# Kernel optimization log

Hardware: AMD Instinct MI355X
Metric: run time of the kernel (lower is better)

The kernel has to match this reference:

```python
import jax, jax.numpy as jnp
import numpy as np

# Model dims
T0 = 2048      # tokens (batch*seq flattened)
D = 2048       # hidden_size
E = 256        # n_routed_experts
K = 8          # num_experts_per_tok
G = 8          # expert groups
EG = 32        # experts per group
R = 64         # tucker rank
I = 1408       # moe_intermediate_size


def setup_inputs() -> dict:
    key = jax.random.key(0)
    ks = jax.random.split(key, 12)
    f = lambda k, s: jax.random.normal(k, s, dtype=jnp.float32) * 0.02
    return {
        "hidden_states": jax.random.normal(ks[0], (T0, D), dtype=jnp.float32),
        "w_gate": f(ks[1], (D, E)),
        # Tucker factors per group: shared in-factor A, per-expert core C, shared out-factor B
        "A_gate": f(ks[2], (G, D, R)), "C_gate": f(ks[3], (G, EG, R, R)), "B_gate": f(ks[4], (G, R, I)),
        "A_up":   f(ks[5], (G, D, R)), "C_up":   f(ks[6], (G, EG, R, R)), "B_up":   f(ks[7], (G, R, I)),
        "A_down": f(ks[8], (G, I, R)), "C_down": f(ks[9], (G, EG, R, R)), "B_down": f(ks[10], (G, R, D)),
    }


def _tucker(x, A, C, B, inner):
    # x: [T, d_in], A: [d_in, R], C: [EG, R, R] gathered per-token, B: [R, d_out]
    h1 = x @ A                                    # [T, R]
    h2 = jnp.einsum('tr,trs->ts', h1, C[inner])   # per-token expert core
    return h2 @ B                                 # [T, d_out]


def reference(hidden_states, w_gate, A_gate, C_gate, B_gate,
              A_up, C_up, B_up, A_down, C_down, B_down):
    # Router: softmax in fp32, top-k, renormalize
    logits = hidden_states @ w_gate                              # [T0, E]
    probs = jax.nn.softmax(logits.astype(jnp.float32), axis=-1)
    rw, sel = jax.lax.top_k(probs, K)                            # [T0, K]
    rw = (rw / rw.sum(axis=-1, keepdims=True)).astype(hidden_states.dtype)

    idx = sel.reshape(-1)          # [T0*K] expert ids of dispatched rows
    gid = idx // EG                # group id
    inner = idx % EG               # expert within group
    x = jnp.repeat(hidden_states, K, axis=0)   # repeat_interleave dispatch [T0*K, D]

    out = jnp.zeros_like(x)
    for g in range(G):             # static loop over 8 structurally distinct groups
        m = (gid == g)[:, None]
        xg = jnp.where(m, x, 0.0)  # masked dispatch (zeros flow to zero through the MLP)
        go = _tucker(xg, A_gate[g], C_gate[g], B_gate[g], inner)
        uo = _tucker(xg, A_up[g],   C_up[g],   B_up[g],   inner)
        inter = jax.nn.silu(go) * uo
        do = _tucker(inter, A_down[g], C_down[g], B_down[g], inner)
        out = out + jnp.where(m, do, 0.0)

    # weighted combine
    return (out.reshape(T0, K, D) * rw[..., None]).sum(axis=1)
```

## Files before the change

### kernel.cpp

```cpp
#include <hip/hip_runtime.h>
#include <math.h>

constexpr int T0n = 2048;
constexpr int Dn  = 2048;
constexpr int En  = 256;
constexpr int Gn  = 8;
constexpr int EGn = 32;
constexpr int Rn  = 64;
constexpr int In  = 1408;

constexpr int NROWS = T0n * 8;
constexpr int SEGCAP = NROWS;
constexpr int KS_R = 4;

typedef __attribute__((ext_vector_type(8))) short s8v;
typedef __attribute__((ext_vector_type(4))) float f4v;
typedef __attribute__((ext_vector_type(4))) int i4v;
#define MFMA16(a, b, c) __builtin_amdgcn_mfma_f32_16x16x32_bf16(a, b, c, 0, 0, 0)
#define MFMAI8(a, b, c) __builtin_amdgcn_mfma_i32_16x16x64_i8(a, b, c, 0, 0, 0)

__device__ __forceinline__ unsigned short f2bf(float x) {
  unsigned int u = __float_as_uint(x);
  unsigned int r = (u + 0x7FFFu + ((u >> 16) & 1u)) >> 16;
  return (unsigned short)r;
}

struct TD { const float* src; unsigned short* dst; int rows, cols, nbx, per_batch, base; };
struct TD9 { TD t[9]; };

__global__ __launch_bounds__(256) void k_tcvt9(TD9 D) {
  __shared__ float tbuf[32][33];
  int id = blockIdx.x;
  int ti = 0;
#pragma unroll
  for (int i = 1; i < 9; ++i) ti = (id >= D.t[i].base) ? i : ti;
  TD d = D.t[ti];
  int local = id - d.base;
  int bz = local / d.per_batch;
  int rem = local - bz * d.per_batch;
  int by = rem / d.nbx;
  int bx = rem - by * d.nbx;

  size_t boff = (size_t)bz * d.rows * d.cols;
  const float* src = d.src + boff;
  unsigned short* dst = d.dst + boff;
  int c0 = bx * 32, r0 = by * 32;
  int tx = threadIdx.x & 31, ty = threadIdx.x >> 5;
  for (int i = ty; i < 32; i += 8)
    tbuf[i][tx] = src[(size_t)(r0 + i) * d.cols + c0 + tx];
  __syncthreads();
  for (int i = ty; i < 32; i += 8)
    dst[(size_t)(c0 + i) * d.rows + r0 + tx] = f2bf(tbuf[tx][i]);
}

__device__ __forceinline__ int4 limbs4(float v, double sc) {
  double d = (double)v * sc;
  d = fmin(fmax(d, -2.0e9), 2.0e9);
  int x = __double2int_rn(d);
  int l0 = (int)(signed char)(x & 0xff); x = (x - l0) >> 8;
  int l1 = (int)(signed char)(x & 0xff); x = (x - l1) >> 8;
  int l2 = (int)(signed char)(x & 0xff); x = (x - l2) >> 8;
  return make_int4(l0, l1, l2, x);
}

__global__ __launch_bounds__(256) void k_quant_h(
    const float* __restrict__ H, char* __restrict__ hq) {
  const size_t PL = (size_t)T0n * Dn;
  size_t i = (size_t)blockIdx.x * 256 + threadIdx.x;
  float4 v = *(const float4*)&H[i * 4];
  int4 a = limbs4(v.x, 268435456.0);
  int4 b = limbs4(v.y, 268435456.0);
  int4 c = limbs4(v.z, 268435456.0);
  int4 d = limbs4(v.w, 268435456.0);
  unsigned int p0 = (a.x & 0xff) | ((b.x & 0xff) << 8) | ((c.x & 0xff) << 16) | ((unsigned)(d.x & 0xff) << 24);
  unsigned int p1 = (a.y & 0xff) | ((b.y & 0xff) << 8) | ((c.y & 0xff) << 16) | ((unsigned)(d.y & 0xff) << 24);
  unsigned int p2 = (a.z & 0xff) | ((b.z & 0xff) << 8) | ((c.z & 0xff) << 16) | ((unsigned)(d.z & 0xff) << 24);
  unsigned int p3 = (a.w & 0xff) | ((b.w & 0xff) << 8) | ((c.w & 0xff) << 16) | ((unsigned)(d.w & 0xff) << 24);
  *(unsigned int*)&hq[0 * PL + i * 4] = p0;
  *(unsigned int*)&hq[1 * PL + i * 4] = p1;
  *(unsigned int*)&hq[2 * PL + i * 4] = p2;
  *(unsigned int*)&hq[3 * PL + i * 4] = p3;
}

__global__ __launch_bounds__(256) void k_quant_wT(
    const float* __restrict__ W, char* __restrict__ wqT) {
  __shared__ float tb[32][33];
  const size_t PL = (size_t)En * Dn;
  int kb = blockIdx.x * 32, nb = blockIdx.y * 32;
  int tx = threadIdx.x & 31, ty = threadIdx.x >> 5;
  for (int i = ty; i < 32; i += 8)
    tb[i][tx] = W[(size_t)(kb + i) * En + nb + tx];
  __syncthreads();
  for (int i = ty; i < 32; i += 8) {
    int4 l = limbs4(tb[tx][i], 8589934592.0);
    size_t off = (size_t)(nb + i) * Dn + kb + tx;
    wqT[0 * PL + off] = (char)l.x;
    wqT[1 * PL + off] = (char)l.y;
    wqT[2 * PL + off] = (char)l.z;
    wqT[3 * PL + off] = (char)l.w;
  }
}

__global__ __launch_bounds__(256) void k_router_i8(
    const char* __restrict__ hq, const char* __restrict__ wqT,
    float* __restrict__ part) {
  __shared__ __align__(16) char Asl[4][64][80];
  __shared__ __align__(16) char Bsl[4][64][80];
  const int n0 = blockIdx.x * 64, m0 = blockIdx.y * 64;
  const int kc = blockIdx.z;
  const int tid = threadIdx.x;
  const int w = tid >> 6, ln = tid & 63;
  const int quad = ln >> 4, lane16 = ln & 15;

  const char* ha = hq + ((size_t)w * T0n + m0 + ln) * Dn;
  const char* ba = wqT + ((size_t)w * En + n0 + ln) * Dn;

  i4v acc[4][5] = {};

  const int kbeg = kc * (Dn / KS_R);
  for (int k0 = kbeg; k0 < kbeg + Dn / KS_R; k0 += 64) {
#pragma unroll
    for (int q = 0; q < 4; ++q) {
      *(uint4*)&Asl[w][ln][q * 16] = *(const uint4*)&ha[k0 + q * 16];
      *(uint4*)&Bsl[w][ln][q * 16] = *(const uint4*)&ba[k0 + q * 16];
    }
    __syncthreads();
    i4v b0 = *(const i4v*)&Bsl[0][w * 16 + lane16][quad * 16];
    i4v b1 = *(const i4v*)&Bsl[1][w * 16 + lane16][quad * 16];
    i4v b2 = *(const i4v*)&Bsl[2][w * 16 + lane16][quad * 16];
    i4v b3 = *(const i4v*)&Bsl[3][w * 16 + lane16][quad * 16];
#pragma unroll
    for (int mt = 0; mt < 4; ++mt) {
      i4v a0 = *(const i4v*)&Asl[0][mt * 16 + lane16][quad * 16];
      i4v a1 = *(const i4v*)&Asl[1][mt * 16 + lane16][quad * 16];
      i4v a2 = *(const i4v*)&Asl[2][mt * 16 + lane16][quad * 16];
      i4v a3 = *(const i4v*)&Asl[3][mt * 16 + lane16][quad * 16];
      acc[mt][0] = MFMAI8(a0, b2, acc[mt][0]);
      acc[mt][0] = MFMAI8(a1, b1, acc[mt][0]);
      acc[mt][0] = MFMAI8(a2, b0, acc[mt][0]);
      acc[mt][1] = MFMAI8(a0, b3, acc[mt][1]);
      acc[mt][1] = MFMAI8(a1, b2, acc[mt][1]);
      acc[mt][1] = MFMAI8(a2, b1, acc[mt][1]);
      acc[mt][1] = MFMAI8(a3, b0, acc[mt][1]);
      acc[mt][2] = MFMAI8(a1, b3, acc[mt][2]);
      acc[mt][2] = MFMAI8(a2, b2, acc[mt][2]);
      acc[mt][2] = MFMAI8(a3, b1, acc[mt][2]);
      acc[mt][3] = MFMAI8(a2, b3, acc[mt][3]);
      acc[mt][3] = MFMAI8(a3, b2, acc[mt][3]);
      acc[mt][4] = MFMAI8(a3, b3, acc[mt][4]);
    }
    __syncthreads();
  }

  float* prow = part + (size_t)kc * T0n * En;
#pragma unroll
  for (int mt = 0; mt < 4; ++mt)
#pragma unroll
    for (int r = 0; r < 4; ++r) {
      int row = m0 + mt * 16 + quad * 4 + r;
      int col = n0 + w * 16 + lane16;
      double v = (double)acc[mt][0][r] * 0x1p-45 +
                 (double)acc[mt][1][r] * 0x1p-37 +
                 (double)acc[mt][2][r] * 0x1p-29 +
                 (double)acc[mt][3][r] * 0x1p-21 +
                 (double)acc[mt][4][r] * 0x1p-13;
      prow[(size_t)row * En + col] = (float)v;
    }
}

__global__ __launch_bounds__(256) void k_topk(
    const float* __restrict__ part, int* __restrict__ sel,
    float* __restrict__ rw, int* __restrict__ cnt_e) {
  const int wid = threadIdx.x >> 6, ln = threadIdx.x & 63;
  const int t = blockIdx.x * 4 + wid;

  double v[4];
#pragma unroll
  for (int j = 0; j < 4; ++j) {
    double s = 0.0;
#pragma unroll
    for (int kc = 0; kc < KS_R; ++kc)
      s += (double)part[((size_t)kc * T0n + t) * En + ln + 64 * j];
    v[j] = s;
  }

  float topv[8];
  int topi[8];
#pragma unroll
  for (int k = 0; k < 8; ++k) {
    double bv = v[0]; int bi = ln;
#pragma unroll
    for (int j = 1; j < 4; ++j) {
      int cand = ln + 64 * j;
      if (v[j] > bv || (v[j] == bv && cand < bi)) { bv = v[j]; bi = cand; }
    }
#pragma unroll
    for (int off = 32; off > 0; off >>= 1) {
      double ov = __shfl_xor(bv, off);
      int oi = __shfl_xor(bi, off);
      if (ov > bv || (ov == bv && oi < bi)) { bv = ov; bi = oi; }
    }
    topv[k] = (float)bv; topi[k] = bi;
    if ((bi & 63) == ln) v[bi >> 6] = -1e300;
  }

  if (ln < 8) {
    float m = topv[0];
    float ssum = 0.f;
#pragma unroll
    for (int k = 0; k < 8; ++k) ssum += expf(topv[k] - m);
    rw[t * 8 + ln] = expf(topv[ln] - m) / ssum;
    sel[t * 8 + ln] = topi[ln];
    atomicAdd(&cnt_e[topi[ln]], 1);
  }
}

__global__ __launch_bounds__(256) void k_scan(
    const int* __restrict__ cnt_e, int* __restrict__ off_e,
    int* __restrict__ cur_e, int* __restrict__ grp_n) {
  __shared__ int c[256];
  int tid = threadIdx.x;
  c[tid] = cnt_e[tid];
  __syncthreads();
  int g = tid >> 5, ei = tid & 31;
  int run = 0;
  for (int i = 0; i < ei; ++i) run += c[(g << 5) + i];
  off_e[tid] = g * SEGCAP + run;
  cur_e[tid] = g * SEGCAP + run;
  if (ei == 31) grp_n[g] = run + c[tid];
}

__global__ void k_scatter(const int* __restrict__ sel, int* __restrict__ cur_e,
                          int* __restrict__ rseg) {
  int i = blockIdx.x * 256 + threadIdx.x;
  int e = sel[i];
  int pos = atomicAdd(&cur_e[e], 1);
  rseg[pos] = i;
}

__global__ __launch_bounds__(512) void k_h1_mfma(
    const float* __restrict__ H,
    const unsigned short* __restrict__ AgT, const unsigned short* __restrict__ AuT,
    unsigned short* __restrict__ h1gb, unsigned short* __restrict__ h1ub) {
  const int t0 = blockIdx.x * 64;
  const int g = blockIdx.y;
  const unsigned short* Wg = AgT + (size_t)g * Rn * Dn;
  const unsigned short* Wu = AuT + (size_t)g * Rn * Dn;

  __shared__ unsigned short As[64 * 72];
  __shared__ unsigned short Bg_l[64 * 72];
  __shared__ unsigned short Bu_l[64 * 72];
  const int tid = threadIdx.x;
  const int w = tid >> 6, ln = tid & 63;
  const int path = w >> 2, ws = w & 3;
  const int quad = ln >> 4, lane16 = ln & 15;
  const int j = tid >> 3, q = (tid & 7) * 8;

  f4v S[4] = {};

  for (int k0 = 0; k0 < Dn; k0 += 64) {
    {
      float4 v0 = *(const float4*)&H[(size_t)(t0 + j) * Dn + k0 + q];
      float4 v1 = *(const float4*)&H[(size_t)(t0 + j) * Dn + k0 + q + 4];
      ushort4 o0, o1;
      o0.x = f2bf(v0.x); o0.y = f2bf(v0.y); o0.z = f2bf(v0.z); o0.w = f2bf(v0.w);
      o1.x = f2bf(v1.x); o1.y = f2bf(v1.y); o1.z = f2bf(v1.z); o1.w = f2bf(v1.w);
      *(ushort4*)&As[j * 72 + q] = o0;
      *(ushort4*)&As[j * 72 + q + 4] = o1;
      *(uint4*)&Bg_l[j * 72 + q] = *(const uint4*)&Wg[(size_t)j * Dn + k0 + q];
      *(uint4*)&Bu_l[j * 72 + q] = *(const uint4*)&Wu[(size_t)j * Dn + k0 + q];
    }
    __syncthreads();
    const unsigned short* Bl = path ? Bu_l : Bg_l;
#pragma unroll
    for (int kk = 0; kk < 2; ++kk) {
      s8v a = *(const s8v*)&As[(ws * 16 + lane16) * 72 + kk * 32 + quad * 8];
#pragma unroll
      for (int nt = 0; nt < 4; ++nt) {
        s8v b = *(const s8v*)&Bl[(nt * 16 + lane16) * 72 + kk * 32 + quad * 8];
        S[nt] = MFMA16(a, b, S[nt]);
      }
    }
    __syncthreads();
  }
  unsigned short* out = path ? h1ub : h1gb;
#pragma unroll
  for (int nt = 0; nt < 4; ++nt)
#pragma unroll
    for (int r = 0; r < 4; ++r) {
      int row = t0 + ws * 16 + quad * 4 + r;
      int col = g * 64 + nt * 16 + lane16;
      out[(size_t)row * (Gn * Rn) + col] = f2bf(S[nt][r]);
    }
}

__global__ __launch_bounds__(512) void k_core_gu(
    const unsigned short* __restrict__ h1gb, const unsigned short* __restrict__ h1ub,
    const unsigned short* __restrict__ CgT, const unsigned short* __restrict__ CuT,
    const int* __restrict__ rseg, const int* __restrict__ off_e,
    const int* __restrict__ cnt_e,
    unsigned short* __restrict__ h2gb, unsigned short* __restrict__ h2ub) {
  const int e = blockIdx.x;
  const int ne = cnt_e[e];
  if (ne == 0) return;
  const int g = e >> 5;
  const int base = off_e[e];
  __shared__ unsigned short Cg_l[64 * 72];
  __shared__ unsigned short Cu_l[64 * 72];
  __shared__ unsigned short Ags[64 * 72];
  __shared__ unsigned short Aus[64 * 72];
  __shared__ int rids[64];
  const int tid = threadIdx.x;
  const int w = tid >> 6, ln = tid & 63;
  const int path = w >> 2, ws = w & 3;
  const int quad = ln >> 4, lane16 = ln & 15;
  const int j = tid >> 3, q = (tid & 7) * 8;
  {
    const unsigned short* cg = CgT + (size_t)e * (Rn * Rn);
    const unsigned short* cu = CuT + (size_t)e * (Rn * Rn);
    *(uint4*)&Cg_l[j * 72 + q] = *(const uint4*)&cg[j * 64 + q];
    *(uint4*)&Cu_l[j * 72 + q] = *(const uint4*)&cu[j * 64 + q];
  }
  const int ntile = (ne + 63) >> 6;
  for (int it = 0; it < ntile; ++it) {
    int mi = it * 64 + j;
    int rid = (mi < ne) ? rseg[base + mi] : -1;
    if ((tid & 7) == 0) rids[j] = rid;
    uint4 zg = {0, 0, 0, 0}, zu = {0, 0, 0, 0};
    if (rid >= 0) {
      zg = *(const uint4*)&h1gb[(size_t)(rid >> 3) * (Gn * Rn) + g * 64 + q];
      zu = *(const uint4*)&h1ub[(size_t)(rid >> 3) * (Gn * Rn) + g * 64 + q];
    }
    *(uint4*)&Ags[j * 72 + q] = zg;
    *(uint4*)&Aus[j * 72 + q] = zu;
    __syncthreads();
    const unsigned short* Al = path ? Aus : Ags;
    const unsigned short* Cl = path ? Cu_l : Cg_l;
    f4v S[4] = {};
#pragma unroll
    for (int kk = 0; kk < 2; ++kk) {
      s8v a = *(const s8v*)&Al[(ws * 16 + lane16) * 72 + kk * 32 + quad * 8];
#pragma unroll
      for (int nt = 0; nt < 4; ++nt) {
        s8v b = *(const s8v*)&Cl[(nt * 16 + lane16) * 72 + kk * 32 + quad * 8];
        S[nt] = MFMA16(a, b, S[nt]);
      }
    }
    unsigned short* out = path ? h2ub : h2gb;
#pragma unroll
    for (int nt = 0; nt < 4; ++nt)
#pragma unroll
      for (int r = 0; r < 4; ++r) {
        int rid2 = rids[ws * 16 + quad * 4 + r];
        if (rid2 >= 0)
          out[(size_t)rid2 * 64 + nt * 16 + lane16] = f2bf(S[nt][r]);
      }
    __syncthreads();
  }
}

__global__ __launch_bounds__(256) void k_expand_mfma(
    const unsigned short* __restrict__ h2gb, const unsigned short* __restrict__ h2ub,
    const unsigned short* __restrict__ BgT, const unsigned short* __restrict__ BuT,
    const unsigned short* __restrict__ AdT,
    const int* __restrict__ rseg, const int* __restrict__ grp_n,
    float* __restrict__ h1d) {
  const int g = blockIdx.z;
  const int ng = grp_n[g];
  const int m0 = blockIdx.y * 128;
  if (m0 >= ng) return;
  const int c_beg = blockIdx.x * 6;
  const int c_end = min(22, c_beg + 6);

  __shared__ unsigned short Hg_l[128 * 72];
  __shared__ unsigned short Hu_l[128 * 72];
  __shared__ unsigned short Bg_l[64 * 72];
  __shared__ unsigned short Bu_l[64 * 72];
  __shared__ unsigned short Ad_l[64 * 72];
  __shared__ int rids[128];

  const int tid = threadIdx.x;
  const int w = tid >> 6, ln = tid & 63;
  const int quad = ln >> 4, lane16 = ln & 15;

  if (tid < 128) rids[tid] = (m0 + tid < ng) ? rseg[g * SEGCAP + m0 + tid] : -1;
  __syncthreads();
#pragma unroll
  for (int i = 0; i < 4; ++i) {
    int c = tid + i * 256;
    int row = c >> 3, cc = (c & 7) * 8;
    int rid = rids[row];
    uint4 zg = {0, 0, 0, 0}, zu = {0, 0, 0, 0};
    if (rid >= 0) {
      zg = *(const uint4*)&h2gb[(size_t)rid * 64 + cc];
      zu = *(const uint4*)&h2ub[(size_t)rid * 64 + cc];
    }
    *(uint4*)&Hg_l[row * 72 + cc] = zg;
    *(uint4*)&Hu_l[row * 72 + cc] = zu;
  }

  const unsigned short* Bg_base = BgT + (size_t)g * In * Rn;
  const unsigned short* Bu_base = BuT + (size_t)g * In * Rn;
  const unsigned short* Ad_base = AdT + (size_t)g * Rn * In;

  f4v P[2][4] = {};

  for (int c = c_beg; c < c_end; ++c) {
    const int i0 = c * 64;
#pragma unroll
    for (int i = 0; i < 2; ++i) {
      int cq = tid + i * 256;
      int row = cq >> 3, co = (cq & 7) * 8;
      *(uint4*)&Bg_l[row * 72 + co] = *(const uint4*)&Bg_base[(size_t)(i0 + row) * Rn + co];
      *(uint4*)&Bu_l[row * 72 + co] = *(const uint4*)&Bu_base[(size_t)(i0 + row) * Rn + co];
      *(uint4*)&Ad_l[row * 72 + co] = *(const uint4*)&Ad_base[(size_t)row * In + i0 + co];
    }
    __syncthreads();

    f4v Sg[2][4] = {}, Su[2][4] = {};
#pragma unroll
    for (int kk = 0; kk < 2; ++kk) {
      s8v ag[2], au[2], bg[4], bu[4];
#pragma unroll
      for (int mt = 0; mt < 2; ++mt) {
        ag[mt] = *(const s8v*)&Hg_l[(w * 32 + mt * 16 + lane16) * 72 + kk * 32 + quad * 8];
        au[mt] = *(const s8v*)&Hu_l[(w * 32 + mt * 16 + lane16) * 72 + kk * 32 + quad * 8];
      }
#pragma unroll
      for (int nt = 0; nt < 4; ++nt) {
        bg[nt] = *(const s8v*)&Bg_l[(nt * 16 + lane16) * 72 + kk * 32 + quad * 8];
        bu[nt] = *(const s8v*)&Bu_l[(nt * 16 + lane16) * 72 + kk * 32 + quad * 8];
      }
#pragma unroll
      for (int mt = 0; mt < 2; ++mt)
#pragma unroll
        for (int nt = 0; nt < 4; ++nt) {
          Sg[mt][nt] = MFMA16(ag[mt], bg[nt], Sg[mt][nt]);
          Su[mt][nt] = MFMA16(au[mt], bu[nt], Su[mt][nt]);
        }
    }
    __syncthreads();
    {
      unsigned short* ibuf = (w < 2) ? Bg_l : Bu_l;
#pragma unroll
      for (int mt = 0; mt < 2; ++mt)
#pragma unroll
        for (int nt = 0; nt < 4; ++nt)
#pragma unroll
          for (int r = 0; r < 4; ++r) {
            float sg = Sg[mt][nt][r];
            float v = sg / (1.f + __expf(-sg)) * Su[mt][nt][r];
            int row = (w * 32 + mt * 16 + quad * 4 + r) & 63;
            ibuf[row * 72 + nt * 16 + lane16] = f2bf(v);
          }
    }
    __syncthreads();
#pragma unroll
    for (int kk = 0; kk < 2; ++kk) {
      s8v ai[2], bd[4];
#pragma unroll
      for (int mt = 0; mt < 2; ++mt) {
        const unsigned short* src = (w < 2) ? Bg_l : Bu_l;
        int arow = (w * 32 + mt * 16 + lane16) & 63;
        ai[mt] = *(const s8v*)&src[arow * 72 + kk * 32 + quad * 8];
      }
#pragma unroll
      for (int nt = 0; nt < 4; ++nt)
        bd[nt] = *(const s8v*)&Ad_l[(nt * 16 + lane16) * 72 + kk * 32 + quad * 8];
#pragma unroll
      for (int mt = 0; mt < 2; ++mt)
#pragma unroll
        for (int nt = 0; nt < 4; ++nt)
          P[mt][nt] = MFMA16(ai[mt], bd[nt], P[mt][nt]);
    }
    __syncthreads();
  }

#pragma unroll
  for (int mt = 0; mt < 2; ++mt)
#pragma unroll
    for (int nt = 0; nt < 4; ++nt)
#pragma unroll
      for (int r = 0; r < 4; ++r) {
        int lrow = w * 32 + mt * 16 + quad * 4 + r;
        int rid = rids[lrow];
        if (rid >= 0)
          atomicAdd(&h1d[(size_t)rid * 64 + nt * 16 + lane16], P[mt][nt][r]);
      }
}

__global__ __launch_bounds__(512) void k_core_down(
    const float* __restrict__ h1d, const unsigned short* __restrict__ CdT,
    const float* __restrict__ rw,
    const int* __restrict__ rseg, const int* __restrict__ off_e,
    const int* __restrict__ cnt_e,
    float* __restrict__ y) {
  const int e = blockIdx.x;
  const int ne = cnt_e[e];
  if (ne == 0) return;
  const int g = e >> 5;
  const int base = off_e[e];
  __shared__ unsigned short Bd_l[64 * 72];
  __shared__ unsigned short Ad_l[128 * 72];
  __shared__ int rids[128];
  const int tid = threadIdx.x;
  const int w = tid >> 6, ln = tid & 63;
  const int quad = ln >> 4, lane16 = ln & 15;
  {
    int j = tid >> 3, q = (tid & 7) * 8;
    const unsigned short* cd = CdT + (size_t)e * (Rn * Rn);
    *(uint4*)&Bd_l[j * 72 + q] = *(const uint4*)&cd[j * 64 + q];
  }
  const int gj = tid >> 2, gq = (tid & 3) * 16;
  const int ntile = (ne + 127) >> 7;
  for (int it = 0; it < ntile; ++it) {
    int mi = it * 128 + gj;
    int rid = (mi < ne) ? rseg[base + mi] : -1;
    if ((tid & 3) == 0) rids[gj] = rid;
#pragma unroll
    for (int i = 0; i < 4; ++i) {
      int kb = gq + i * 4;
      float4 vd = {0.f, 0.f, 0.f, 0.f};
      if (rid >= 0) vd = *(const float4*)&h1d[(size_t)rid * 64 + kb];
      ushort4 od;
      od.x = f2bf(vd.x); od.y = f2bf(vd.y); od.z = f2bf(vd.z); od.w = f2bf(vd.w);
      *(ushort4*)&Ad_l[gj * 72 + kb] = od;
    }
    __syncthreads();
    f4v Sd[4] = {};
#pragma unroll
    for (int kk = 0; kk < 2; ++kk) {
      s8v ad = *(const s8v*)&Ad_l[(w * 16 + lane16) * 72 + kk * 32 + quad * 8];
#pragma unroll
      for (int nt = 0; nt < 4; ++nt) {
        s8v bd = *(const s8v*)&Bd_l[(nt * 16 + lane16) * 72 + kk * 32 + quad * 8];
        Sd[nt] = MFMA16(ad, bd, Sd[nt]);
      }
    }
#pragma unroll
    for (int nt = 0; nt < 4; ++nt)
#pragma unroll
      for (int r = 0; r < 4; ++r) {
        int rid2 = rids[w * 16 + quad * 4 + r];
        if (rid2 >= 0) {
          float wgt = rw[rid2];
          atomicAdd(&y[(size_t)(rid2 >> 3) * (Gn * Rn) + g * 64 + nt * 16 + lane16],
                    wgt * Sd[nt][r]);
        }
      }
    __syncthreads();
  }
}

__global__ __launch_bounds__(256) void k_combine(
    const float* __restrict__ y, const unsigned short* __restrict__ BdT,
    float* __restrict__ outp) {
  const int t0 = blockIdx.y * 128, n0 = blockIdx.x * 128;
  __shared__ unsigned short As[128 * 72];
  __shared__ unsigned short Bs[128 * 72];
  const int tid = threadIdx.x;
  const int w = tid >> 6, ln = tid & 63;
  const int quad = ln >> 4, lane16 = ln & 15;
  const int mbase = (w >> 1) * 64, nbase = (w & 1) * 64;

  f4v acc[4][4] = {};

  for (int k0 = 0; k0 < Gn * Rn; k0 += 64) {
#pragma unroll
    for (int i = 0; i < 8; ++i) {
      int c = tid + i * 256;
      int row = c >> 4, cc = (c & 15) * 4;
      float4 v = *(const float4*)&y[(size_t)(t0 + row) * (Gn * Rn) + k0 + cc];
      ushort4 o;
      o.x = f2bf(v.x); o.y = f2bf(v.y); o.z = f2bf(v.z); o.w = f2bf(v.w);
      *(ushort4*)&As[row * 72 + cc] = o;
    }
#pragma unroll
    for (int i = 0; i < 4; ++i) {
      int c = tid + i * 256;
      int row = c >> 3, cc = (c & 7) * 8;
      *(uint4*)&Bs[row * 72 + cc] = *(const uint4*)&BdT[(size_t)(n0 + row) * (Gn * Rn) + k0 + cc];
    }
    __syncthreads();
#pragma unroll
    for (int kk = 0; kk < 2; ++kk) {
      s8v a[4], b[4];
#pragma unroll
      for (int mt = 0; mt < 4; ++mt)
        a[mt] = *(const s8v*)&As[(mbase + mt * 16 + lane16) * 72 + kk * 32 + quad * 8];
#pragma unroll
      for (int nt = 0; nt < 4; ++nt)
        b[nt] = *(const s8v*)&Bs[(nbase + nt * 16 + lane16) * 72 + kk * 32 + quad * 8];
#pragma unroll
      for (int mt = 0; mt < 4; ++mt)
#pragma unroll
        for (int nt = 0; nt < 4; ++nt)
          acc[mt][nt] = MFMA16(a[mt], b[nt], acc[mt][nt]);
    }
    __syncthreads();
  }
#pragma unroll
  for (int mt = 0; mt < 4; ++mt)
#pragma unroll
    for (int nt = 0; nt < 4; ++nt)
#pragma unroll
      for (int r = 0; r < 4; ++r)
        outp[(size_t)(t0 + mbase + mt * 16 + quad * 4 + r) * Dn +
             n0 + nbase + nt * 16 + lane16] = acc[mt][nt][r];
}

extern "C" void kernel_launch(void* const* d_in, const int* in_sizes, int n_in,
                              void* d_out, int out_size, void* d_ws, size_t ws_size,
                              hipStream_t stream) {
  const float* hidden = (const float*)d_in[0];
  const float* w_gate = (const float*)d_in[1];
  const float* A_gate = (const float*)d_in[2];
  const float* C_gate = (const float*)d_in[3];
  const float* B_gate = (const float*)d_in[4];
  const float* A_up   = (const float*)d_in[5];
  const float* C_up   = (const float*)d_in[6];
  const float* B_up   = (const float*)d_in[7];
  const float* A_down = (const float*)d_in[8];
  const float* C_down = (const float*)d_in[9];
  const float* B_down = (const float*)d_in[10];
  float* out = (float*)d_out;

  char* base = (char*)d_ws;
  size_t o = 0;
  unsigned short* h2gb = (unsigned short*)(base + o); o += (size_t)NROWS * Rn * 2;
  unsigned short* h2ub = (unsigned short*)(base + o); o += (size_t)NROWS * Rn * 2;
  unsigned short* AgT  = (unsigned short*)(base + o); o += (size_t)Gn * Rn * Dn * 2;
  unsigned short* AuT  = (unsigned short*)(base + o); o += (size_t)Gn * Rn * Dn * 2;
  unsigned short* BgT  = (unsigned short*)(base + o); o += (size_t)Gn * In * Rn * 2;
  unsigned short* BuT  = (unsigned short*)(base + o); o += (size_t)Gn * In * Rn * 2;
  unsigned short* AdT  = (unsigned short*)(base + o); o += (size_t)Gn * Rn * In * 2;
  unsigned short* BdT  = (unsigned short*)(base + o); o += (size_t)Dn * Gn * Rn * 2;
  unsigned short* CgT  = (unsigned short*)(base + o); o += (size_t)En * Rn * Rn * 2;
  unsigned short* CuT  = (unsigned short*)(base + o); o += (size_t)En * Rn * Rn * 2;
  unsigned short* CdT  = (unsigned short*)(base + o); o += (size_t)En * Rn * Rn * 2;
  unsigned short* h1gb = (unsigned short*)(base + o); o += (size_t)T0n * Gn * Rn * 2;
  unsigned short* h1ub = (unsigned short*)(base + o); o += (size_t)T0n * Gn * Rn * 2;
  float* h1d = (float*)(base + o); o += (size_t)NROWS * Rn * 4;
  float* y   = (float*)(base + o); o += (size_t)T0n * Gn * Rn * 4;
  float* rwp = (float*)(base + o); o += (size_t)NROWS * 4;
  int* sel   = (int*)(base + o); o += (size_t)NROWS * 4;
  int* rseg  = (int*)(base + o); o += (size_t)Gn * SEGCAP * 4;
  int* cnt_e = (int*)(base + o); o += En * 4;
  int* off_e = (int*)(base + o); o += En * 4;
  int* cur_e = (int*)(base + o); o += En * 4;
  int* grp_n = (int*)(base + o); o += Gn * 4;
  float* part = (float*)base;
  char* hq  = base + (size_t)KS_R * T0n * En * 4;
  char* wqT = hq + (size_t)4 * T0n * Dn;

  hipMemsetAsync(cnt_e, 0, En * sizeof(int), stream);

  k_quant_h<<<T0n * Dn / 1024, 256, 0, stream>>>(hidden, hq);
  k_quant_wT<<<dim3(Dn / 32, En / 32), 256, 0, stream>>>(w_gate, wqT);
  k_router_i8<<<dim3(En / 64, T0n / 64, KS_R), 256, 0, stream>>>(hq, wqT, part);
  k_topk<<<T0n / 4, 256, 0, stream>>>(part, sel, rwp, cnt_e);
  k_scan<<<1, 256, 0, stream>>>(cnt_e, off_e, cur_e, grp_n);
  k_scatter<<<NROWS / 256, 256, 0, stream>>>(sel, cur_e, rseg);

  hipMemsetAsync(h1d, 0, (size_t)NROWS * Rn * sizeof(float), stream);
  hipMemsetAsync(y,   0, (size_t)T0n * Gn * Rn * sizeof(float), stream);

  {
    TD9 D;
    D.t[0] = {A_gate, AgT, Dn, Rn, Rn / 32, (Rn / 32) * (Dn / 32), 0};
    D.t[1] = {A_up,   AuT, Dn, Rn, Rn / 32, (Rn / 32) * (Dn / 32), 1024};
    D.t[2] = {B_gate, BgT, Rn, In, In / 32, (In / 32) * (Rn / 32), 2048};
    D.t[3] = {B_up,   BuT, Rn, In, In / 32, (In / 32) * (Rn / 32), 2752};
    D.t[4] = {A_down, AdT, In, Rn, Rn / 32, (Rn / 32) * (In / 32), 3456};
    D.t[5] = {B_down, BdT, Gn * Rn, Dn, Dn / 32, (Dn / 32) * (Gn * Rn / 32), 4160};
    D.t[6] = {C_gate, CgT, Rn, Rn, 2, 4, 5184};
    D.t[7] = {C_up,   CuT, Rn, Rn, 2, 4, 6208};
    D.t[8] = {C_down, CdT, Rn, Rn, 2, 4, 7232};
    k_tcvt9<<<8256, 256, 0, stream>>>(D);
  }

  k_h1_mfma<<<dim3(T0n / 64, Gn), 512, 0, stream>>>(hidden, AgT, AuT, h1gb, h1ub);
  k_core_gu<<<En, 512, 0, stream>>>(h1gb, h1ub, CgT, CuT,
                                    rseg, off_e, cnt_e, h2gb, h2ub);
  k_expand_mfma<<<dim3(4, NROWS / 128, Gn), 256, 0, stream>>>(
      h2gb, h2ub, BgT, BuT, AdT, rseg, grp_n, h1d);
  k_core_down<<<En, 512, 0, stream>>>(h1d, CdT, rwp,
                                      rseg, off_e, cnt_e, y);
  k_combine<<<dim3(Dn / 128, T0n / 128), 256, 0, stream>>>(y, BdT, out);
}
```

Baseline: 333.4 us.

## Keep h2 fragments in registers and use per-wave intermediate LDS buffers

```diff
diff --git a/kernel.cpp b/kernel.cpp
--- a/kernel.cpp
+++ b/kernel.cpp
@@ -372,11 +372,10 @@
   const int c_beg = blockIdx.x * 6;
   const int c_end = min(22, c_beg + 6);
 
-  __shared__ unsigned short Hg_l[128 * 72];
-  __shared__ unsigned short Hu_l[128 * 72];
   __shared__ unsigned short Bg_l[64 * 72];
   __shared__ unsigned short Bu_l[64 * 72];
   __shared__ unsigned short Ad_l[64 * 72];
+  __shared__ unsigned short inter_l[4][32 * 72];
   __shared__ int rids[128];
 
   const int tid = threadIdx.x;
@@ -385,24 +384,28 @@
 
   if (tid < 128) rids[tid] = (m0 + tid < ng) ? rseg[g * SEGCAP + m0 + tid] : -1;
   __syncthreads();
-#pragma unroll
-  for (int i = 0; i < 4; ++i) {
-    int c = tid + i * 256;
-    int row = c >> 3, cc = (c & 7) * 8;
-    int rid = rids[row];
-    uint4 zg = {0, 0, 0, 0}, zu = {0, 0, 0, 0};
-    if (rid >= 0) {
-      zg = *(const uint4*)&h2gb[(size_t)rid * 64 + cc];
-      zu = *(const uint4*)&h2ub[(size_t)rid * 64 + cc];
-    }
-    *(uint4*)&Hg_l[row * 72 + cc] = zg;
-    *(uint4*)&Hu_l[row * 72 + cc] = zu;
+
+  s8v ag[2][2], au[2][2];
+#pragma unroll
+  for (int mt = 0; mt < 2; ++mt) {
+    int rid = rids[w * 32 + mt * 16 + lane16];
+#pragma unroll
+    for (int kk = 0; kk < 2; ++kk) {
+      s8v zg = {}, zu = {};
+      if (rid >= 0) {
+        zg = *(const s8v*)&h2gb[(size_t)rid * 64 + kk * 32 + quad * 8];
+        zu = *(const s8v*)&h2ub[(size_t)rid * 64 + kk * 32 + quad * 8];
+      }
+      ag[mt][kk] = zg;
+      au[mt][kk] = zu;
+    }
   }
 
   const unsigned short* Bg_base = BgT + (size_t)g * In * Rn;
   const unsigned short* Bu_base = BuT + (size_t)g * In * Rn;
   const unsigned short* Ad_base = AdT + (size_t)g * Rn * In;
 
+  unsigned short* ib = &inter_l[w][0];
   f4v P[2][4] = {};
 
   for (int c = c_beg; c < c_end; ++c) {
@@ -420,12 +423,7 @@
     f4v Sg[2][4] = {}, Su[2][4] = {};
 #pragma unroll
     for (int kk = 0; kk < 2; ++kk) {
-      s8v ag[2], au[2], bg[4], bu[4];
-#pragma unroll
-      for (int mt = 0; mt < 2; ++mt) {
-        ag[mt] = *(const s8v*)&Hg_l[(w * 32 + mt * 16 + lane16) * 72 + kk * 32 + quad * 8];
-        au[mt] = *(const s8v*)&Hu_l[(w * 32 + mt * 16 + lane16) * 72 + kk * 32 + quad * 8];
-      }
+      s8v bg[4], bu[4];
 #pragma unroll
       for (int nt = 0; nt < 4; ++nt) {
         bg[nt] = *(const s8v*)&Bg_l[(nt * 16 + lane16) * 72 + kk * 32 + quad * 8];
@@ -435,35 +433,29 @@
       for (int mt = 0; mt < 2; ++mt)
 #pragma unroll
         for (int nt = 0; nt < 4; ++nt) {
-          Sg[mt][nt] = MFMA16(ag[mt], bg[nt], Sg[mt][nt]);
-          Su[mt][nt] = MFMA16(au[mt], bu[nt], Su[mt][nt]);
+          Sg[mt][nt] = MFMA16(ag[mt][kk], bg[nt], Sg[mt][nt]);
+          Su[mt][nt] = MFMA16(au[mt][kk], bu[nt], Su[mt][nt]);
         }
     }
-    __syncthreads();
-    {
-      unsigned short* ibuf = (w < 2) ? Bg_l : Bu_l;
-#pragma unroll
-      for (int mt = 0; mt < 2; ++mt)
-#pragma unroll
-        for (int nt = 0; nt < 4; ++nt)
-#pragma unroll
-          for (int r = 0; r < 4; ++r) {
-            float sg = Sg[mt][nt][r];
-            float v = sg / (1.f + __expf(-sg)) * Su[mt][nt][r];
-            int row = (w * 32 + mt * 16 + quad * 4 + r) & 63;
-            ibuf[row * 72 + nt * 16 + lane16] = f2bf(v);
-          }
-    }
-    __syncthreads();
+
+#pragma unroll
+    for (int mt = 0; mt < 2; ++mt)
+#pragma unroll
+      for (int nt = 0; nt < 4; ++nt)
+#pragma unroll
+        for (int r = 0; r < 4; ++r) {
+          float sg = Sg[mt][nt][r];
+          float v = sg / (1.f + __expf(-sg)) * Su[mt][nt][r];
+          ib[(mt * 16 + quad * 4 + r) * 72 + nt * 16 + lane16] = f2bf(v);
+        }
+    asm volatile("s_waitcnt lgkmcnt(0)" ::: "memory");
+
 #pragma unroll
     for (int kk = 0; kk < 2; ++kk) {
       s8v ai[2], bd[4];
 #pragma unroll
-      for (int mt = 0; mt < 2; ++mt) {
-        const unsigned short* src = (w < 2) ? Bg_l : Bu_l;
-        int arow = (w * 32 + mt * 16 + lane16) & 63;
-        ai[mt] = *(const s8v*)&src[arow * 72 + kk * 32 + quad * 8];
-      }
+      for (int mt = 0; mt < 2; ++mt)
+        ai[mt] = *(const s8v*)&ib[(mt * 16 + lane16) * 72 + kk * 32 + quad * 8];
 #pragma unroll
       for (int nt = 0; nt < 4; ++nt)
         bd[nt] = *(const s8v*)&Ad_l[(nt * 16 + lane16) * 72 + kk * 32 + quad * 8];
```

Result: no change. 329.8 us (-1.1%).
